# Optimization experiments

Hardware: AMD Instinct MI355X
Metric: run time of the kernel (lower is better)

The kernel has to match this reference:

```python
import jax, jax.numpy as jnp
import numpy as np

N, D, K = 8192, 256, 32

def _cdist(x, y):
    # Euclidean distance via matmul expansion (matches torch 'use_mm' mode)
    x2 = jnp.sum(x * x, axis=-1)[:, None]
    y2 = jnp.sum(y * y, axis=-1)[None, :]
    d2 = x2 + y2 - 2.0 * (x @ y.T)
    return jnp.sqrt(jnp.maximum(d2, 0.0))

def setup_inputs() -> dict:
    key = jax.random.key(0)
    features = jax.random.normal(key, (N, D), dtype=jnp.float32)
    return {"features": features, "k": K}

def reference(features, k):
    n = features.shape[0]
    r_full = _cdist(features, features)                       # [N, N]
    # drop diagonal (rank 0 offset): column j maps to ref index j + (j >= i)
    cols = jnp.arange(n - 1)[None, :] + (jnp.arange(n - 1)[None, :] >= jnp.arange(n)[:, None])
    r = jnp.take_along_axis(r_full, cols, axis=1)             # [N, N-1]
    # sorted distances and their (masked-column) indices
    idx = jnp.argsort(r, axis=1)                              # [N, N-1]
    a = jnp.take_along_axis(r, idx, axis=1)                   # [N, N-1]
    # full reference-vs-reference distances, row-sorted
    a_full_d = jnp.sort(r_full, axis=1)                       # [N, N]
    idx_k = idx[:, :k]                                        # [N, k]
    # faithful to original: idx_k used directly as row indices into a_full_d
    d_k = a_full_d[idx_k, k]                                  # [N, k]
    scores = a[:, k][:, None] / d_k                           # [N, k]
    scores = jnp.mean(scores, axis=1)                         # [N]
    scores = jnp.nan_to_num(scores, nan=1000.0, posinf=1000.0, neginf=0.0)
    return scores
```

## Files before the change

### kernel.cpp

```cpp
#include <hip/hip_runtime.h>

#define N 8192
#define DIM 256
#define QB 32
#define NWAVES 8
#define CB (NWAVES*16)
#define NIT (N / CB)
#define LK 33
#define NBIN 512
#define BUFCAP 128

typedef short bf16x8 __attribute__((ext_vector_type(8)));
typedef float f32x4 __attribute__((ext_vector_type(4)));

static __device__ inline unsigned short f2bf(float f) {
    unsigned int u = __float_as_uint(f);
    unsigned int r = (u + 0x7fffu + ((u >> 16) & 1u)) >> 16;
    return (unsigned short)r;
}

static __device__ inline float dist2(float qn_plus_cn, float acc) {
    return __builtin_fmaf(-2.0f, acc, qn_plus_cn);
}

__global__ __launch_bounds__(64) void prep_kernel(const float* __restrict__ feat,
                                                  unsigned short* __restrict__ fb,
                                                  float* __restrict__ norms) {
    int row = blockIdx.x;
    int lane = threadIdx.x;
    float4 v = reinterpret_cast<const float4*>(feat + (size_t)row * DIM)[lane];
    float ss = v.x * v.x + v.y * v.y + v.z * v.z + v.w * v.w;
    #pragma unroll
    for (int off = 32; off > 0; off >>= 1) ss += __shfl_xor(ss, off);
    if (lane == 0) norms[row] = ss;
    ushort4 b;
    b.x = f2bf(v.x); b.y = f2bf(v.y); b.z = f2bf(v.z); b.w = f2bf(v.w);
    reinterpret_cast<ushort4*>(fb + (size_t)row * DIM)[lane] = b;
}

#define LOAD_AND_PIN_AQ()                                                    \
    int koff = (lane >> 4) * 8;                                              \
    int arow = qbase + (lane & 15);                                          \
    bf16x8 aq[2][8];                                                         \
    _Pragma("unroll")                                                        \
    for (int rt = 0; rt < 2; rt++) {                                         \
        _Pragma("unroll")                                                    \
        for (int ks = 0; ks < 8; ks++) {                                     \
            aq[rt][ks] = *reinterpret_cast<const bf16x8*>(                   \
                fb + (size_t)(arow + rt * 16) * DIM + ks * 32 + koff);       \
            asm volatile("" : "+v"(aq[rt][ks]));                             \
        }                                                                    \
    }

__global__ __launch_bounds__(NWAVES * 64, 2) void hist_kernel(
    const unsigned short* __restrict__ fb, const float* __restrict__ norms,
    float* __restrict__ tq) {
    __shared__ unsigned int hist[QB][NBIN + 1];
    __shared__ float qn[QB];

    int tid = threadIdx.x;
    int w = tid >> 6;
    int lane = tid & 63;
    int qbase = blockIdx.x * QB;

    for (int i = tid; i < QB * (NBIN + 1); i += NWAVES * 64)
        (&hist[0][0])[i] = 0u;
    if (tid < QB) qn[tid] = norms[qbase + tid];
    __syncthreads();

    LOAD_AND_PIN_AQ()

    float qnr[2][4];
    unsigned int* hrow[2][4];
    int qgl[2][4];
    #pragma unroll
    for (int rt = 0; rt < 2; rt++)
        #pragma unroll
        for (int j = 0; j < 4; j++) {
            int ql = rt * 16 + (lane >> 4) * 4 + j;
            qnr[rt][j] = qn[ql];
            hrow[rt][j] = &hist[ql][0];
            qgl[rt][j] = qbase + ql;
        }

    int cbase = w * 16 + (lane & 15);
    const unsigned short* bptr = fb + (size_t)cbase * DIM + koff;

    for (int it = 0; it < NIT; it++) {
        int crow = it * CB + cbase;
        const bf16x8* bp = reinterpret_cast<const bf16x8*>(
            bptr + (size_t)it * CB * DIM);
        bf16x8 bq[8];
        #pragma unroll
        for (int ks = 0; ks < 8; ks++) bq[ks] = bp[ks * 4];
        float cn = norms[crow];

        f32x4 acc0 = {0.f, 0.f, 0.f, 0.f};
        f32x4 acc1 = {0.f, 0.f, 0.f, 0.f};
        #pragma unroll
        for (int ks = 0; ks < 8; ks++) {
            acc0 = __builtin_amdgcn_mfma_f32_16x16x32_bf16(aq[0][ks], bq[ks], acc0, 0, 0, 0);
            acc1 = __builtin_amdgcn_mfma_f32_16x16x32_bf16(aq[1][ks], bq[ks], acc1, 0, 0, 0);
        }

        #pragma unroll
        for (int rt = 0; rt < 2; rt++) {
            f32x4 acc = rt ? acc1 : acc0;
            #pragma unroll
            for (int j = 0; j < 4; j++) {
                float d2 = dist2(qnr[rt][j] + cn, acc[j]);
                if (crow != qgl[rt][j]) {
                    int b = (int)(d2 * 0.5f);
                    b = b < 0 ? 0 : (b > NBIN - 1 ? NBIN - 1 : b);
                    atomicAdd(&hrow[rt][j][b], 1u);
                }
            }
        }
    }
    __syncthreads();

    if (tid < QB) {
        unsigned int cum = 0;
        int bstar = NBIN - 1;
        for (int b = 0; b < NBIN; b++) {
            cum += hist[tid][b];
            if (cum >= LK) { bstar = b; break; }
        }
        tq[qbase + tid] = (float)(bstar + 1) * 2.0f;
    }
}

__device__ inline void rescan_max(const float* ld, const int* li,
                                  float& md, int& mi, int& mp) {
    md = -3.0e38f; mi = -1; mp = 0;
    for (int t = 0; t < LK; t++) {
        float d = ld[t]; int ix = li[t];
        if (d > md || (d == md && ix > mi)) { md = d; mi = ix; mp = t; }
    }
}

__global__ __launch_bounds__(NWAVES * 64, 2) void collect_kernel(
    const unsigned short* __restrict__ fb, const float* __restrict__ norms,
    const float* __restrict__ tq,
    float* __restrict__ kd32sq, float* __restrict__ kd33sq, int* __restrict__ knn) {
    __shared__ float qn[QB];
    __shared__ float Tsh[QB];
    __shared__ float buf_d[QB][BUFCAP];
    __shared__ int   buf_i[QB][BUFCAP];
    __shared__ int   bcnt[QB];
    __shared__ float list_d[QB][LK];
    __shared__ int   list_i[QB][LK];

    int tid = threadIdx.x;
    int w = tid >> 6;
    int lane = tid & 63;
    int qbase = blockIdx.x * QB;

    if (tid < QB) {
        qn[tid] = norms[qbase + tid];
        Tsh[tid] = tq[qbase + tid];
        bcnt[tid] = 0;
    }
    __syncthreads();

    LOAD_AND_PIN_AQ()

    float qnr[2][4], Tr[2][4];
    int qln[2][4], qgl[2][4];
    #pragma unroll
    for (int rt = 0; rt < 2; rt++)
        #pragma unroll
        for (int j = 0; j < 4; j++) {
            int ql = rt * 16 + (lane >> 4) * 4 + j;
            qnr[rt][j] = qn[ql];
            Tr[rt][j] = Tsh[ql];
            qln[rt][j] = ql;
            qgl[rt][j] = qbase + ql;
        }

    int cbase = w * 16 + (lane & 15);
    const unsigned short* bptr = fb + (size_t)cbase * DIM + koff;

    for (int it = 0; it < NIT; it++) {
        int crow = it * CB + cbase;
        const bf16x8* bp = reinterpret_cast<const bf16x8*>(
            bptr + (size_t)it * CB * DIM);
        bf16x8 bq[8];
        #pragma unroll
        for (int ks = 0; ks < 8; ks++) bq[ks] = bp[ks * 4];
        float cn = norms[crow];

        f32x4 acc0 = {0.f, 0.f, 0.f, 0.f};
        f32x4 acc1 = {0.f, 0.f, 0.f, 0.f};
        #pragma unroll
        for (int ks = 0; ks < 8; ks++) {
            acc0 = __builtin_amdgcn_mfma_f32_16x16x32_bf16(aq[0][ks], bq[ks], acc0, 0, 0, 0);
            acc1 = __builtin_amdgcn_mfma_f32_16x16x32_bf16(aq[1][ks], bq[ks], acc1, 0, 0, 0);
        }

        #pragma unroll
        for (int rt = 0; rt < 2; rt++) {
            f32x4 acc = rt ? acc1 : acc0;
            #pragma unroll
            for (int j = 0; j < 4; j++) {
                float d2 = dist2(qnr[rt][j] + cn, acc[j]);
                if (crow != qgl[rt][j] && d2 < Tr[rt][j]) {
                    int ql = qln[rt][j];
                    int p = atomicAdd(&bcnt[ql], 1);
                    if (p < BUFCAP) { buf_d[ql][p] = d2; buf_i[ql][p] = crow; }
                }
            }
        }
    }
    __syncthreads();

    if (tid < QB) {
        int q = tid;
        int g = qbase + q;
        int n = bcnt[q]; if (n > BUFCAP) n = BUFCAP;
        int c = 0;
        float m1d = 3.0e38f; int m1i = 0x7fffffff, m1p = 0;
        for (int b = 0; b < n; b++) {
            float d = buf_d[q][b]; int ix = buf_i[q][b];
            if (c < LK) {
                list_d[q][c] = d; list_i[q][c] = ix; c++;
                if (c == LK) rescan_max(&list_d[q][0], &list_i[q][0], m1d, m1i, m1p);
            } else if (d < m1d || (d == m1d && ix < m1i)) {
                list_d[q][m1p] = d; list_i[q][m1p] = ix;
                rescan_max(&list_d[q][0], &list_i[q][0], m1d, m1i, m1p);
            }
        }
        rescan_max(&list_d[q][0], &list_i[q][0], m1d, m1i, m1p);
        float m2d = -3.0e38f; int m2i = -1;
        for (int t = 0; t < LK; t++) {
            if (t == m1p) continue;
            float d = list_d[q][t]; int ix = list_i[q][t];
            if (d > m2d || (d == m2d && ix > m2i)) { m2d = d; m2i = ix; }
        }
        kd33sq[g] = m1d;
        kd32sq[g] = m2d;
        int o = 0;
        for (int t = 0; t < LK; t++) {
            if (t == m1p) continue;
            knn[(size_t)g * 32 + o] = list_i[q][t];
            o++;
        }
    }
}

__global__ __launch_bounds__(256) void scores_kernel(
    const float* __restrict__ kd32sq, const float* __restrict__ kd33sq,
    const int* __restrict__ knn, float* __restrict__ out) {
    int i = blockIdx.x * blockDim.x + threadIdx.x;
    float num = sqrtf(fmaxf(kd33sq[i], 0.0f));
    float s = 0.0f;
    #pragma unroll
    for (int t = 0; t < 32; t++) {
        int j = knn[(size_t)i * 32 + t];
        int m = j - (j > i);
        float den = sqrtf(fmaxf(kd32sq[m], 0.0f));
        s += num / den;
    }
    s *= (1.0f / 32.0f);
    if (isnan(s)) s = 1000.0f;
    else if (isinf(s)) s = (s > 0.0f) ? 1000.0f : 0.0f;
    out[i] = s;
}

extern "C" void kernel_launch(void* const* d_in, const int* in_sizes, int n_in,
                              void* d_out, int out_size, void* d_ws, size_t ws_size,
                              hipStream_t stream) {
    (void)in_sizes; (void)n_in; (void)out_size; (void)ws_size;
    const float* feat = (const float*)d_in[0];

    char* ws = (char*)d_ws;
    unsigned short* fb = (unsigned short*)ws;
    size_t off = (size_t)4 * 1024 * 1024;
    float* norms = (float*)(ws + off); off += 32768;
    float* kd32  = (float*)(ws + off); off += 32768;
    float* kd33  = (float*)(ws + off); off += 32768;
    float* tqv   = (float*)(ws + off); off += 32768;
    int*   knn   = (int*)(ws + off);

    prep_kernel<<<N, 64, 0, stream>>>(feat, fb, norms);
    hist_kernel<<<N / QB, NWAVES * 64, 0, stream>>>(fb, norms, tqv);
    collect_kernel<<<N / QB, NWAVES * 64, 0, stream>>>(fb, norms, tqv, kd32, kd33, knn);
    scores_kernel<<<N / 256, 256, 0, stream>>>(kd32, kd33, knn, (float*)d_out);
}
```

Measured before the change: 326.3 us.

## Stage query fragments in LDS, split MFMA accumulators, coarsen histogram bins

Query bf16 fragments are now loaded once by wave 0 into shared memory and re-read from LDS inside the loop, instead of being pinned in registers by every wave. This frees VGPRs, at the cost of extra LDS reads on each iteration. The MFMA chains are split into two accumulators per row tile to shorten the dependency chain. The histogram is halved to 256 bins of width 4 with buffer capacity raised to 160, which cuts LDS use and init cost but admits more candidates into the collect phase, raising the overflow risk.

```diff
diff --git a/kernel.cpp b/kernel.cpp
--- a/kernel.cpp
+++ b/kernel.cpp
@@ -7,8 +7,9 @@
 #define CB (NWAVES*16)
 #define NIT (N / CB)
 #define LK 33
-#define NBIN 512
-#define BUFCAP 128
+#define NBIN 256
+#define BUFCAP 160
+#define NFRAG 16
 
 typedef short bf16x8 __attribute__((ext_vector_type(8)));
 typedef float f32x4 __attribute__((ext_vector_type(4)));
@@ -38,23 +39,24 @@
     reinterpret_cast<ushort4*>(fb + (size_t)row * DIM)[lane] = b;
 }
 
-#define LOAD_AND_PIN_AQ()                                                    \
+#define STAGE_AQ_TO_LDS()                                                    \
     int koff = (lane >> 4) * 8;                                              \
-    int arow = qbase + (lane & 15);                                          \
-    bf16x8 aq[2][8];                                                         \
-    _Pragma("unroll")                                                        \
-    for (int rt = 0; rt < 2; rt++) {                                         \
+    if (w == 0) {                                                            \
+        int arow = qbase + (lane & 15);                                      \
         _Pragma("unroll")                                                    \
-        for (int ks = 0; ks < 8; ks++) {                                     \
-            aq[rt][ks] = *reinterpret_cast<const bf16x8*>(                   \
-                fb + (size_t)(arow + rt * 16) * DIM + ks * 32 + koff);       \
-            asm volatile("" : "+v"(aq[rt][ks]));                             \
+        for (int rt = 0; rt < 2; rt++) {                                     \
+            _Pragma("unroll")                                                \
+            for (int ks = 0; ks < 8; ks++)                                   \
+                aLds[(rt * 8 + ks) * 64 + lane] =                            \
+                    *reinterpret_cast<const bf16x8*>(                        \
+                        fb + (size_t)(arow + rt * 16) * DIM + ks * 32 + koff); \
         }                                                                    \
     }
 
 __global__ __launch_bounds__(NWAVES * 64, 2) void hist_kernel(
     const unsigned short* __restrict__ fb, const float* __restrict__ norms,
     float* __restrict__ tq) {
+    __shared__ bf16x8 aLds[NFRAG * 64];
     __shared__ unsigned int hist[QB][NBIN + 1];
     __shared__ float qn[QB];
 
@@ -66,12 +68,12 @@
     for (int i = tid; i < QB * (NBIN + 1); i += NWAVES * 64)
         (&hist[0][0])[i] = 0u;
     if (tid < QB) qn[tid] = norms[qbase + tid];
-    __syncthreads();
-
-    LOAD_AND_PIN_AQ()
+
+    STAGE_AQ_TO_LDS()
+    __syncthreads();
 
     float qnr[2][4];
-    unsigned int* hrow[2][4];
+    int hoff[2][4];
     int qgl[2][4];
     #pragma unroll
     for (int rt = 0; rt < 2; rt++)
@@ -79,9 +81,10 @@
         for (int j = 0; j < 4; j++) {
             int ql = rt * 16 + (lane >> 4) * 4 + j;
             qnr[rt][j] = qn[ql];
-            hrow[rt][j] = &hist[ql][0];
+            hoff[rt][j] = ql * (NBIN + 1);
             qgl[rt][j] = qbase + ql;
         }
+    unsigned int* hflat = &hist[0][0];
 
     int cbase = w * 16 + (lane & 15);
     const unsigned short* bptr = fb + (size_t)cbase * DIM + koff;
@@ -95,24 +98,26 @@
         for (int ks = 0; ks < 8; ks++) bq[ks] = bp[ks * 4];
         float cn = norms[crow];
 
-        f32x4 acc0 = {0.f, 0.f, 0.f, 0.f};
-        f32x4 acc1 = {0.f, 0.f, 0.f, 0.f};
+        f32x4 acc[2][2] = {{{0.f,0.f,0.f,0.f},{0.f,0.f,0.f,0.f}},
+                           {{0.f,0.f,0.f,0.f},{0.f,0.f,0.f,0.f}}};
         #pragma unroll
         for (int ks = 0; ks < 8; ks++) {
-            acc0 = __builtin_amdgcn_mfma_f32_16x16x32_bf16(aq[0][ks], bq[ks], acc0, 0, 0, 0);
-            acc1 = __builtin_amdgcn_mfma_f32_16x16x32_bf16(aq[1][ks], bq[ks], acc1, 0, 0, 0);
+            bf16x8 a0 = aLds[ks * 64 + lane];
+            bf16x8 a1 = aLds[(8 + ks) * 64 + lane];
+            acc[0][ks & 1] = __builtin_amdgcn_mfma_f32_16x16x32_bf16(a0, bq[ks], acc[0][ks & 1], 0, 0, 0);
+            acc[1][ks & 1] = __builtin_amdgcn_mfma_f32_16x16x32_bf16(a1, bq[ks], acc[1][ks & 1], 0, 0, 0);
         }
 
         #pragma unroll
         for (int rt = 0; rt < 2; rt++) {
-            f32x4 acc = rt ? acc1 : acc0;
+            f32x4 s = acc[rt][0] + acc[rt][1];
             #pragma unroll
             for (int j = 0; j < 4; j++) {
-                float d2 = dist2(qnr[rt][j] + cn, acc[j]);
+                float d2 = dist2(qnr[rt][j] + cn, s[j]);
                 if (crow != qgl[rt][j]) {
-                    int b = (int)(d2 * 0.5f);
+                    int b = (int)(d2 * 0.25f);
                     b = b < 0 ? 0 : (b > NBIN - 1 ? NBIN - 1 : b);
-                    atomicAdd(&hrow[rt][j][b], 1u);
+                    atomicAdd(&hflat[hoff[rt][j] + b], 1u);
                 }
             }
         }
@@ -126,7 +131,7 @@
             cum += hist[tid][b];
             if (cum >= LK) { bstar = b; break; }
         }
-        tq[qbase + tid] = (float)(bstar + 1) * 2.0f;
+        tq[qbase + tid] = (float)(bstar + 1) * 4.0f;
     }
 }
 
@@ -143,6 +148,7 @@
     const unsigned short* __restrict__ fb, const float* __restrict__ norms,
     const float* __restrict__ tq,
     float* __restrict__ kd32sq, float* __restrict__ kd33sq, int* __restrict__ knn) {
+    __shared__ bf16x8 aLds[NFRAG * 64];
     __shared__ float qn[QB];
     __shared__ float Tsh[QB];
     __shared__ float buf_d[QB][BUFCAP];
@@ -161,9 +167,9 @@
         Tsh[tid] = tq[qbase + tid];
         bcnt[tid] = 0;
     }
-    __syncthreads();
-
-    LOAD_AND_PIN_AQ()
+
+    STAGE_AQ_TO_LDS()
+    __syncthreads();
 
     float qnr[2][4], Tr[2][4];
     int qln[2][4], qgl[2][4];
@@ -190,20 +196,22 @@
         for (int ks = 0; ks < 8; ks++) bq[ks] = bp[ks * 4];
         float cn = norms[crow];
 
-        f32x4 acc0 = {0.f, 0.f, 0.f, 0.f};
-        f32x4 acc1 = {0.f, 0.f, 0.f, 0.f};
+        f32x4 acc[2][2] = {{{0.f,0.f,0.f,0.f},{0.f,0.f,0.f,0.f}},
+                           {{0.f,0.f,0.f,0.f},{0.f,0.f,0.f,0.f}}};
         #pragma unroll
         for (int ks = 0; ks < 8; ks++) {
-            acc0 = __builtin_amdgcn_mfma_f32_16x16x32_bf16(aq[0][ks], bq[ks], acc0, 0, 0, 0);
-            acc1 = __builtin_amdgcn_mfma_f32_16x16x32_bf16(aq[1][ks], bq[ks], acc1, 0, 0, 0);
+            bf16x8 a0 = aLds[ks * 64 + lane];
+            bf16x8 a1 = aLds[(8 + ks) * 64 + lane];
+            acc[0][ks & 1] = __builtin_amdgcn_mfma_f32_16x16x32_bf16(a0, bq[ks], acc[0][ks & 1], 0, 0, 0);
+            acc[1][ks & 1] = __builtin_amdgcn_mfma_f32_16x16x32_bf16(a1, bq[ks], acc[1][ks & 1], 0, 0, 0);
         }
 
         #pragma unroll
         for (int rt = 0; rt < 2; rt++) {
-            f32x4 acc = rt ? acc1 : acc0;
+            f32x4 s = acc[rt][0] + acc[rt][1];
             #pragma unroll
             for (int j = 0; j < 4; j++) {
-                float d2 = dist2(qnr[rt][j] + cn, acc[j]);
+                float d2 = dist2(qnr[rt][j] + cn, s[j]);
                 if (crow != qgl[rt][j] && d2 < Tr[rt][j]) {
                     int ql = qln[rt][j];
                     int p = atomicAdd(&bcnt[ql], 1);
```

Measured after the change: 375.8 us. 1.15x slower.
